# Performance work log

Measured on AMD Instinct MI355X. Metric: run time of the kernel, lower is better.

## Reference

```python
import jax, jax.numpy as jnp
import numpy as np

B, T, IN, CELL, OUT = 512, 32, 512, 128, 128


def setup_inputs() -> dict:
    key = jax.random.key(0)
    ks = jax.random.split(key, 6)
    d = IN + CELL
    w = lambda k, shape, fan: jax.random.normal(k, shape, jnp.float32) / np.sqrt(fan).astype(np.float32)
    return {
        "x": jax.random.normal(ks[0], (B, T, IN), jnp.float32),
        "Wf": w(ks[1], (d, CELL), d), "bf": jnp.zeros((CELL,), jnp.float32),
        "Wi1": w(ks[2], (d, CELL), d), "bi1": jnp.zeros((CELL,), jnp.float32),
        "Wi2": w(ks[3], (d, CELL), d), "bi2": jnp.zeros((CELL,), jnp.float32),
        "Wo": w(ks[4], (d, CELL), d), "bo": jnp.zeros((CELL,), jnp.float32),
        "Wc": w(ks[5], (CELL, OUT), CELL), "bc": jnp.zeros((OUT,), jnp.float32),
    }


def reference(x, Wf, bf, Wi1, bi1, Wi2, bi2, Wo, bo, Wc, bc):
    # Faithful to MyLSTM.forward: loop runs x.shape[1] times; each iteration
    # concatenates the FULL [B,T,CELL] cell_state with the FULL [B,T,IN] x
    # (x is never sliced per step). Only the last iteration's output matters,
    # but we carry it through the scan to match the loop structure exactly.
    Tn = x.shape[1]
    c0 = jnp.zeros(x.shape[:2] + (Wf.shape[1],), x.dtype)
    out0 = jnp.zeros(x.shape[:2] + (Wc.shape[1],), x.dtype)

    def step(carry, _):
        c, _prev_out = carry
        inp = jnp.concatenate([c, x], axis=-1)  # [B,T,CELL+IN]
        f = jax.nn.sigmoid(inp @ Wf + bf)
        c = c * f + jax.nn.sigmoid(inp @ Wi1 + bi1) * jnp.tanh(inp @ Wi2 + bi2)
        o = jax.nn.sigmoid(inp @ Wo + bo) * jnp.tanh(c)
        out = jax.nn.softmax(o @ Wc + bc, axis=2)  # out_features != 1 branch
        return (c, out), None

    (c, out), _ = jax.lax.scan(step, (c0, out0), None, length=Tn)
    return out, c
```

## Files before the change

### kernel.cpp

```cpp
#include <hip/hip_runtime.h>
#include <stdint.h>

#define ROWS  16384
#define CELL  128
#define INF   512
#define RPB   32
#define NSTEP 32

typedef _Float16 f16x8 __attribute__((ext_vector_type(8)));
typedef _Float16 f16x4 __attribute__((ext_vector_type(4)));
typedef float    f32x16 __attribute__((ext_vector_type(16)));

#define MFMA32(a, b, c) __builtin_amdgcn_mfma_f32_32x32x16_f16((a), (b), (c), 0, 0, 0)

#define AOFF  0
#define XOFF  65536
#define WCOFF 327680
#define WSTOT 344064

__device__ __forceinline__ unsigned short f2h_bits(float f) {
  _Float16 h = (_Float16)f;
  return *(unsigned short*)&h;
}
__device__ __forceinline__ float sig_f(float z) {
  return __builtin_amdgcn_rcpf(1.f + __expf(-z));
}
__device__ __forceinline__ float tanh_f(float z) {
  return 1.f - 2.f * __builtin_amdgcn_rcpf(__expf(2.f * z) + 1.f);
}

__global__ __launch_bounds__(256) void prep_kernel(
    const float* __restrict__ Wf, const float* __restrict__ Wi1,
    const float* __restrict__ Wi2, const float* __restrict__ Wo,
    const float* __restrict__ Wc, unsigned short* __restrict__ ws) {
  int id = blockIdx.x * blockDim.x + threadIdx.x;
  if (id >= WSTOT) return;
  const float* Wg[4] = {Wf, Wi1, Wi2, Wo};
  if (id < XOFF) {
    int g = id >> 14, r = id & 16383;
    int j = r & 7, lane = (r >> 3) & 63, tile = r >> 9;
    int nb = tile & 3, ks = tile >> 2;
    int k = ks * 16 + ((lane >> 5) << 3) + j;
    int n = nb * 32 + (lane & 31);
    ws[id] = f2h_bits(Wg[g][k * CELL + n]);
  } else if (id < WCOFF) {
    int t = id - XOFF;
    int g = t >> 16, r = t & 65535;
    int j = r & 7, lane = (r >> 3) & 63, tile = r >> 9;
    int nb = tile & 3, ks = tile >> 2;
    int k = ks * 16 + ((lane >> 5) << 3) + j;
    int n = nb * 32 + (lane & 31);
    ws[id] = f2h_bits(Wg[g][(CELL + k) * CELL + n]);
  } else {
    int r = id - WCOFF;
    int j = r & 7, lane = (r >> 3) & 63, tile = r >> 9;
    int nb = tile & 3, ks = tile >> 2;
    int k = ks * 16 + ((lane >> 5) << 3) + j;
    int n = nb * 32 + (lane & 31);
    ws[id] = f2h_bits(Wc[k * CELL + n]);
  }
}

__global__ __launch_bounds__(256, 2) void lstm_kernel(
    const float* __restrict__ x,
    const float* __restrict__ bf_, const float* __restrict__ bi1,
    const float* __restrict__ bi2, const float* __restrict__ bo,
    const float* __restrict__ bc,
    const unsigned short* __restrict__ ws, float* __restrict__ out) {

  __shared__ union {
    _Float16 xs[32][264];
    struct {
      _Float16 o[32][136];
      float    s[32][132];
    } ep;
  } uS;
  __shared__ _Float16 cF[2][32][136];
  __shared__ float    uo[32][132];

  const int tid  = threadIdx.x;
  const int lane = tid & 63;
  const int w    = tid >> 6;
  const int n    = lane & 31;
  const int l5   = lane >> 5;
  const int col  = w * 32 + n;
  const int r0   = blockIdx.x * RPB;

  const _Float16* Aw  = (const _Float16*)ws + AOFF;
  const _Float16* Xw  = (const _Float16*)ws + XOFF;
  const _Float16* Wcw = (const _Float16*)ws + WCOFF;

  f32x16 u[4];
#pragma unroll
  for (int g = 0; g < 4; ++g)
#pragma unroll
    for (int i = 0; i < 16; ++i) u[g][i] = 0.f;

  const float* xbase = x + (size_t)r0 * INF;
#pragma unroll 1
  for (int ch = 0; ch < 2; ++ch) {
    if (ch) __syncthreads();
#pragma unroll
    for (int i = 0; i < 8; ++i) {
      int flat = tid + i * 256;
      int row = flat >> 6, c4 = flat & 63;
      const float4 v = ((const float4*)(xbase + (size_t)row * INF + ch * 256))[c4];
      f16x4 h = {(_Float16)v.x, (_Float16)v.y, (_Float16)v.z, (_Float16)v.w};
      *(f16x4*)&uS.xs[row][c4 * 4] = h;
    }
    __syncthreads();
#pragma unroll 2
    for (int ks8 = 0; ks8 < 16; ++ks8) {
      f16x8 a = *(const f16x8*)&uS.xs[n][ks8 * 16 + l5 * 8];
      int ks = ch * 16 + ks8;
#pragma unroll
      for (int g = 0; g < 4; ++g) {
        f16x8 b = *(const f16x8*)(Xw + g * 65536 + ((ks * 4 + w) * 64 + lane) * 8);
        u[g] = MFMA32(a, b, u[g]);
      }
    }
  }
  {
    float b0 = bf_[col], b1 = bi1[col], b2 = bi2[col], b3 = bo[col];
#pragma unroll
    for (int reg = 0; reg < 16; ++reg) {
      u[0][reg] += b0; u[1][reg] += b1; u[2][reg] += b2;
      int r = (reg & 3) + 8 * (reg >> 2) + 4 * l5;
      uo[r][col] = u[3][reg] + b3;
    }
  }

  f16x8 wr[3][8];
#pragma unroll
  for (int g = 0; g < 3; ++g)
#pragma unroll
    for (int ks = 0; ks < 8; ++ks)
      wr[g][ks] = *(const f16x8*)(Aw + g * 16384 + ((ks * 4 + w) * 64 + lane) * 8);

  f32x16 cr;
#pragma unroll
  for (int reg = 0; reg < 16; ++reg) {
    float ig = sig_f(u[1][reg]);
    float gg = tanh_f(u[2][reg]);
    float c0 = ig * gg;
    cr[reg] = c0;
    int r = (reg & 3) + 8 * (reg >> 2) + 4 * l5;
    cF[0][r][col] = (_Float16)c0;
  }
  __syncthreads();

#pragma unroll 1
  for (int t = 1; t < NSTEP - 1; ++t) {
    const int rb = (t + 1) & 1, wb = t & 1;
    f16x8 a[8];
#pragma unroll
    for (int ks = 0; ks < 8; ++ks)
      a[ks] = *(const f16x8*)&cF[rb][n][ks * 16 + l5 * 8];
    f32x16 zf = u[0], zi1 = u[1], zi2 = u[2];
#pragma unroll
    for (int ks = 0; ks < 8; ++ks) {
      zf  = MFMA32(a[ks], wr[0][ks], zf);
      zi1 = MFMA32(a[ks], wr[1][ks], zi1);
      zi2 = MFMA32(a[ks], wr[2][ks], zi2);
    }
#pragma unroll
    for (int reg = 0; reg < 16; ++reg) {
      float fg = sig_f(zf[reg]);
      float ig = sig_f(zi1[reg]);
      float gg = tanh_f(zi2[reg]);
      float cn = fmaf(cr[reg], fg, ig * gg);
      cr[reg] = cn;
      int r = (reg & 3) + 8 * (reg >> 2) + 4 * l5;
      cF[wb][r][col] = (_Float16)cn;
    }
    __syncthreads();
  }

  {
    f16x8 a[8];
#pragma unroll
    for (int ks = 0; ks < 8; ++ks)
      a[ks] = *(const f16x8*)&cF[0][n][ks * 16 + l5 * 8];
    f32x16 zf = u[0], zi1 = u[1], zi2 = u[2], zo;
#pragma unroll
    for (int reg = 0; reg < 16; ++reg) {
      int r = (reg & 3) + 8 * (reg >> 2) + 4 * l5;
      zo[reg] = uo[r][col];
    }
#pragma unroll
    for (int ks = 0; ks < 8; ++ks) {
      f16x8 bo_frag = *(const f16x8*)(Aw + 3 * 16384 + ((ks * 4 + w) * 64 + lane) * 8);
      zf  = MFMA32(a[ks], wr[0][ks], zf);
      zi1 = MFMA32(a[ks], wr[1][ks], zi1);
      zi2 = MFMA32(a[ks], wr[2][ks], zi2);
      zo  = MFMA32(a[ks], bo_frag, zo);
    }
    __syncthreads();
#pragma unroll
    for (int reg = 0; reg < 16; ++reg) {
      float fg = sig_f(zf[reg]);
      float ig = sig_f(zi1[reg]);
      float gg = tanh_f(zi2[reg]);
      float cn = fmaf(cr[reg], fg, ig * gg);
      cr[reg] = cn;
      float ov = sig_f(zo[reg]) * tanh_f(cn);
      int r = (reg & 3) + 8 * (reg >> 2) + 4 * l5;
      uS.ep.o[r][col] = (_Float16)ov;
    }
    __syncthreads();
  }

  {
    f32x16 sacc;
#pragma unroll
    for (int i = 0; i < 16; ++i) sacc[i] = 0.f;
#pragma unroll
    for (int ks = 0; ks < 8; ++ks) {
      f16x8 a = *(const f16x8*)&uS.ep.o[n][ks * 16 + l5 * 8];
      f16x8 b = *(const f16x8*)(Wcw + ((ks * 4 + w) * 64 + lane) * 8);
      sacc = MFMA32(a, b, sacc);
    }
    float bv = bc[col];
#pragma unroll
    for (int reg = 0; reg < 16; ++reg) {
      int r = (reg & 3) + 8 * (reg >> 2) + 4 * l5;
      uS.ep.s[r][col] = sacc[reg] + bv;
    }
    __syncthreads();

#pragma unroll
    for (int rr = 0; rr < 8; ++rr) {
      int r = w * 8 + rr;
      float v0 = uS.ep.s[r][lane];
      float v1 = uS.ep.s[r][lane + 64];
      float m = fmaxf(v0, v1);
#pragma unroll
      for (int off = 32; off; off >>= 1) m = fmaxf(m, __shfl_xor(m, off, 64));
      float e0 = __expf(v0 - m), e1 = __expf(v1 - m);
      float sm = e0 + e1;
#pragma unroll
      for (int off = 32; off; off >>= 1) sm += __shfl_xor(sm, off, 64);
      float inv = __builtin_amdgcn_rcpf(sm);
      size_t base = (size_t)(r0 + r) * 128;
      out[base + lane]      = e0 * inv;
      out[base + lane + 64] = e1 * inv;
    }

#pragma unroll
    for (int reg = 0; reg < 16; ++reg) {
      int r = (reg & 3) + 8 * (reg >> 2) + 4 * l5;
      out[(size_t)ROWS * 128 + (size_t)(r0 + r) * 128 + col] = cr[reg];
    }
  }
}

extern "C" void kernel_launch(void* const* d_in, const int* in_sizes, int n_in,
                              void* d_out, int out_size, void* d_ws, size_t ws_size,
                              hipStream_t stream) {
  const float* x   = (const float*)d_in[0];
  const float* Wf  = (const float*)d_in[1];
  const float* bf_ = (const float*)d_in[2];
  const float* Wi1 = (const float*)d_in[3];
  const float* bi1 = (const float*)d_in[4];
  const float* Wi2 = (const float*)d_in[5];
  const float* bi2 = (const float*)d_in[6];
  const float* Wo  = (const float*)d_in[7];
  const float* bo  = (const float*)d_in[8];
  const float* Wc  = (const float*)d_in[9];
  const float* bc  = (const float*)d_in[10];
  unsigned short* ws = (unsigned short*)d_ws;
  float* out = (float*)d_out;

  hipLaunchKernelGGL(prep_kernel, dim3((WSTOT + 255) / 256), dim3(256), 0, stream,
                     Wf, Wi1, Wi2, Wo, Wc, ws);
  hipLaunchKernelGGL(lstm_kernel, dim3(ROWS / RPB), dim3(256), 0, stream,
                     x, bf_, bi1, bi2, bo, bc, ws, out);
}
```

Baseline: 177.4 us.

## Fold exp2 scaling into weights and transpose MFMA operands for vectorized stores

Pre-scales the gate and classifier weights and biases by -log2e or 2*log2e during prep, so activations use raw exp2 and rcp without an extra multiply. Swaps the MFMA operand roles so weights are the A operand and the transposed cell state is B. Each lane's accumulator registers then map to contiguous columns, which allows packed f16x4 and float4 stores to LDS and global memory in place of scalar scattered stores. The uo shared buffer is removed and the output-gate preactivation stays in registers, at the cost of slightly more register pressure and f16 rounding of the scaled weights.

```diff
diff --git a/kernel.cpp b/kernel.cpp
--- a/kernel.cpp
+++ b/kernel.cpp
@@ -7,13 +7,21 @@
 #define RPB   32
 #define NSTEP 32
 
+#define LOG2E 1.4426950408889634f
+
 typedef _Float16 f16x8 __attribute__((ext_vector_type(8)));
 typedef _Float16 f16x4 __attribute__((ext_vector_type(4)));
 typedef float    f32x16 __attribute__((ext_vector_type(16)));
 
 #define MFMA32(a, b, c) __builtin_amdgcn_mfma_f32_32x32x16_f16((a), (b), (c), 0, 0, 0)
 
-#define AOFF  0
+#if __has_builtin(__builtin_amdgcn_exp2f)
+#define EXP2(x) __builtin_amdgcn_exp2f(x)
+#else
+#define EXP2(x) __expf((x) * 0.6931471805599453f)
+#endif
+#define RCP(x) __builtin_amdgcn_rcpf(x)
+
 #define XOFF  65536
 #define WCOFF 327680
 #define WSTOT 344064
@@ -21,12 +29,6 @@
 __device__ __forceinline__ unsigned short f2h_bits(float f) {
   _Float16 h = (_Float16)f;
   return *(unsigned short*)&h;
-}
-__device__ __forceinline__ float sig_f(float z) {
-  return __builtin_amdgcn_rcpf(1.f + __expf(-z));
-}
-__device__ __forceinline__ float tanh_f(float z) {
-  return 1.f - 2.f * __builtin_amdgcn_rcpf(__expf(2.f * z) + 1.f);
 }
 
 __global__ __launch_bounds__(256) void prep_kernel(
@@ -36,28 +38,26 @@
   int id = blockIdx.x * blockDim.x + threadIdx.x;
   if (id >= WSTOT) return;
   const float* Wg[4] = {Wf, Wi1, Wi2, Wo};
+  const float sc[4] = {-LOG2E, -LOG2E, 2.f * LOG2E, -LOG2E};
   if (id < XOFF) {
     int g = id >> 14, r = id & 16383;
-    int j = r & 7, lane = (r >> 3) & 63, tile = r >> 9;
-    int nb = tile & 3, ks = tile >> 2;
+    int w = r >> 12, ks = (r >> 9) & 7, lane = (r >> 3) & 63, j = r & 7;
     int k = ks * 16 + ((lane >> 5) << 3) + j;
-    int n = nb * 32 + (lane & 31);
-    ws[id] = f2h_bits(Wg[g][k * CELL + n]);
+    int n = w * 32 + (lane & 31);
+    ws[id] = f2h_bits(Wg[g][k * CELL + n] * sc[g]);
   } else if (id < WCOFF) {
     int t = id - XOFF;
     int g = t >> 16, r = t & 65535;
-    int j = r & 7, lane = (r >> 3) & 63, tile = r >> 9;
-    int nb = tile & 3, ks = tile >> 2;
+    int w = r >> 14, ks = (r >> 9) & 31, lane = (r >> 3) & 63, j = r & 7;
     int k = ks * 16 + ((lane >> 5) << 3) + j;
-    int n = nb * 32 + (lane & 31);
-    ws[id] = f2h_bits(Wg[g][(CELL + k) * CELL + n]);
+    int n = w * 32 + (lane & 31);
+    ws[id] = f2h_bits(Wg[g][(CELL + k) * CELL + n] * sc[g]);
   } else {
     int r = id - WCOFF;
-    int j = r & 7, lane = (r >> 3) & 63, tile = r >> 9;
-    int nb = tile & 3, ks = tile >> 2;
+    int w = r >> 12, ks = (r >> 9) & 7, lane = (r >> 3) & 63, j = r & 7;
     int k = ks * 16 + ((lane >> 5) << 3) + j;
-    int n = nb * 32 + (lane & 31);
-    ws[id] = f2h_bits(Wc[k * CELL + n]);
+    int n = w * 32 + (lane & 31);
+    ws[id] = f2h_bits(Wc[k * CELL + n] * LOG2E);
   }
 }
 
@@ -75,18 +75,16 @@
       float    s[32][132];
     } ep;
   } uS;
-  __shared__ _Float16 cF[2][32][136];
-  __shared__ float    uo[32][132];
+  __shared__ _Float16 cT[2][32][136];
 
   const int tid  = threadIdx.x;
   const int lane = tid & 63;
   const int w    = tid >> 6;
-  const int n    = lane & 31;
+  const int n31  = lane & 31;
   const int l5   = lane >> 5;
-  const int col  = w * 32 + n;
   const int r0   = blockIdx.x * RPB;
 
-  const _Float16* Aw  = (const _Float16*)ws + AOFF;
+  const _Float16* Aw  = (const _Float16*)ws;
   const _Float16* Xw  = (const _Float16*)ws + XOFF;
   const _Float16* Wcw = (const _Float16*)ws + WCOFF;
 
@@ -110,24 +108,23 @@
     }
     __syncthreads();
 #pragma unroll 2
-    for (int ks8 = 0; ks8 < 16; ++ks8) {
-      f16x8 a = *(const f16x8*)&uS.xs[n][ks8 * 16 + l5 * 8];
-      int ks = ch * 16 + ks8;
+    for (int ksl = 0; ksl < 16; ++ksl) {
+      f16x8 b = *(const f16x8*)&uS.xs[n31][ksl * 16 + l5 * 8];
+      int ks = ch * 16 + ksl;
 #pragma unroll
       for (int g = 0; g < 4; ++g) {
-        f16x8 b = *(const f16x8*)(Xw + g * 65536 + ((ks * 4 + w) * 64 + lane) * 8);
+        f16x8 a = *(const f16x8*)(Xw + (((g * 4 + w) * 32 + ks) * 64 + lane) * 8);
         u[g] = MFMA32(a, b, u[g]);
       }
     }
   }
-  {
-    float b0 = bf_[col], b1 = bi1[col], b2 = bi2[col], b3 = bo[col];
-#pragma unroll
-    for (int reg = 0; reg < 16; ++reg) {
-      u[0][reg] += b0; u[1][reg] += b1; u[2][reg] += b2;
-      int r = (reg & 3) + 8 * (reg >> 2) + 4 * l5;
-      uo[r][col] = u[3][reg] + b3;
-    }
+#pragma unroll
+  for (int reg = 0; reg < 16; ++reg) {
+    int col = w * 32 + (reg & 3) + 8 * (reg >> 2) + 4 * l5;
+    u[0][reg] += bf_[col] * (-LOG2E);
+    u[1][reg] += bi1[col] * (-LOG2E);
+    u[2][reg] += bi2[col] * (2.f * LOG2E);
+    u[3][reg] += bo[col]  * (-LOG2E);
   }
 
   f16x8 wr[3][8];
@@ -135,96 +132,106 @@
   for (int g = 0; g < 3; ++g)
 #pragma unroll
     for (int ks = 0; ks < 8; ++ks)
-      wr[g][ks] = *(const f16x8*)(Aw + g * 16384 + ((ks * 4 + w) * 64 + lane) * 8);
+      wr[g][ks] = *(const f16x8*)(Aw + (((g * 4 + w) * 8 + ks) * 64 + lane) * 8);
 
   f32x16 cr;
 #pragma unroll
   for (int reg = 0; reg < 16; ++reg) {
-    float ig = sig_f(u[1][reg]);
-    float gg = tanh_f(u[2][reg]);
-    float c0 = ig * gg;
-    cr[reg] = c0;
-    int r = (reg & 3) + 8 * (reg >> 2) + 4 * l5;
-    cF[0][r][col] = (_Float16)c0;
+    float ig = RCP(1.f + EXP2(u[1][reg]));
+    float gg = fmaf(-2.f, RCP(1.f + EXP2(u[2][reg])), 1.f);
+    cr[reg] = ig * gg;
+  }
+#pragma unroll
+  for (int qd = 0; qd < 4; ++qd) {
+    f16x4 p = {(_Float16)cr[qd * 4 + 0], (_Float16)cr[qd * 4 + 1],
+               (_Float16)cr[qd * 4 + 2], (_Float16)cr[qd * 4 + 3]};
+    *(f16x4*)&cT[0][n31][w * 32 + qd * 8 + l5 * 4] = p;
   }
   __syncthreads();
 
 #pragma unroll 1
   for (int t = 1; t < NSTEP - 1; ++t) {
     const int rb = (t + 1) & 1, wb = t & 1;
-    f16x8 a[8];
+    f16x8 b[8];
 #pragma unroll
     for (int ks = 0; ks < 8; ++ks)
-      a[ks] = *(const f16x8*)&cF[rb][n][ks * 16 + l5 * 8];
+      b[ks] = *(const f16x8*)&cT[rb][n31][ks * 16 + l5 * 8];
     f32x16 zf = u[0], zi1 = u[1], zi2 = u[2];
 #pragma unroll
     for (int ks = 0; ks < 8; ++ks) {
-      zf  = MFMA32(a[ks], wr[0][ks], zf);
-      zi1 = MFMA32(a[ks], wr[1][ks], zi1);
-      zi2 = MFMA32(a[ks], wr[2][ks], zi2);
+      zf  = MFMA32(wr[0][ks], b[ks], zf);
+      zi1 = MFMA32(wr[1][ks], b[ks], zi1);
+      zi2 = MFMA32(wr[2][ks], b[ks], zi2);
     }
 #pragma unroll
     for (int reg = 0; reg < 16; ++reg) {
-      float fg = sig_f(zf[reg]);
-      float ig = sig_f(zi1[reg]);
-      float gg = tanh_f(zi2[reg]);
+      float fg = RCP(1.f + EXP2(zf[reg]));
+      float ig = RCP(1.f + EXP2(zi1[reg]));
+      float gg = fmaf(-2.f, RCP(1.f + EXP2(zi2[reg])), 1.f);
+      cr[reg] = fmaf(cr[reg], fg, ig * gg);
+    }
+#pragma unroll
+    for (int qd = 0; qd < 4; ++qd) {
+      f16x4 p = {(_Float16)cr[qd * 4 + 0], (_Float16)cr[qd * 4 + 1],
+                 (_Float16)cr[qd * 4 + 2], (_Float16)cr[qd * 4 + 3]};
+      *(f16x4*)&cT[wb][n31][w * 32 + qd * 8 + l5 * 4] = p;
+    }
+    __syncthreads();
+  }
+
+  {
+    f16x8 b[8];
+#pragma unroll
+    for (int ks = 0; ks < 8; ++ks)
+      b[ks] = *(const f16x8*)&cT[0][n31][ks * 16 + l5 * 8];
+    f32x16 zf = u[0], zi1 = u[1], zi2 = u[2], zo = u[3];
+#pragma unroll
+    for (int ks = 0; ks < 8; ++ks) {
+      f16x8 wof = *(const f16x8*)(Aw + (((3 * 4 + w) * 8 + ks) * 64 + lane) * 8);
+      zf  = MFMA32(wr[0][ks], b[ks], zf);
+      zi1 = MFMA32(wr[1][ks], b[ks], zi1);
+      zi2 = MFMA32(wr[2][ks], b[ks], zi2);
+      zo  = MFMA32(wof, b[ks], zo);
+    }
+    float ovv[16];
+#pragma unroll
+    for (int reg = 0; reg < 16; ++reg) {
+      float fg = RCP(1.f + EXP2(zf[reg]));
+      float ig = RCP(1.f + EXP2(zi1[reg]));
+      float gg = fmaf(-2.f, RCP(1.f + EXP2(zi2[reg])), 1.f);
       float cn = fmaf(cr[reg], fg, ig * gg);
       cr[reg] = cn;
-      int r = (reg & 3) + 8 * (reg >> 2) + 4 * l5;
-      cF[wb][r][col] = (_Float16)cn;
+      float th = fmaf(-2.f, RCP(1.f + EXP2(cn * (2.f * LOG2E))), 1.f);
+      ovv[reg] = RCP(1.f + EXP2(zo[reg])) * th;
+    }
+#pragma unroll
+    for (int qd = 0; qd < 4; ++qd) {
+      f16x4 p = {(_Float16)ovv[qd * 4 + 0], (_Float16)ovv[qd * 4 + 1],
+                 (_Float16)ovv[qd * 4 + 2], (_Float16)ovv[qd * 4 + 3]};
+      *(f16x4*)&uS.ep.o[n31][w * 32 + qd * 8 + l5 * 4] = p;
     }
     __syncthreads();
   }
 
   {
-    f16x8 a[8];
-#pragma unroll
-    for (int ks = 0; ks < 8; ++ks)
-      a[ks] = *(const f16x8*)&cF[0][n][ks * 16 + l5 * 8];
-    f32x16 zf = u[0], zi1 = u[1], zi2 = u[2], zo;
+    f32x16 sa;
+#pragma unroll
+    for (int i = 0; i < 16; ++i) sa[i] = 0.f;
+#pragma unroll
+    for (int ks = 0; ks < 8; ++ks) {
+      f16x8 a = *(const f16x8*)(Wcw + ((w * 8 + ks) * 64 + lane) * 8);
+      f16x8 b = *(const f16x8*)&uS.ep.o[n31][ks * 16 + l5 * 8];
+      sa = MFMA32(a, b, sa);
+    }
 #pragma unroll
     for (int reg = 0; reg < 16; ++reg) {
-      int r = (reg & 3) + 8 * (reg >> 2) + 4 * l5;
-      zo[reg] = uo[r][col];
-    }
-#pragma unroll
-    for (int ks = 0; ks < 8; ++ks) {
-      f16x8 bo_frag = *(const f16x8*)(Aw + 3 * 16384 + ((ks * 4 + w) * 64 + lane) * 8);
-      zf  = MFMA32(a[ks], wr[0][ks], zf);
-      zi1 = MFMA32(a[ks], wr[1][ks], zi1);
-      zi2 = MFMA32(a[ks], wr[2][ks], zi2);
-      zo  = MFMA32(a[ks], bo_frag, zo);
-    }
-    __syncthreads();
-#pragma unroll
-    for (int reg = 0; reg < 16; ++reg) {
-      float fg = sig_f(zf[reg]);
-      float ig = sig_f(zi1[reg]);
-      float gg = tanh_f(zi2[reg]);
-      float cn = fmaf(cr[reg], fg, ig * gg);
-      cr[reg] = cn;
-      float ov = sig_f(zo[reg]) * tanh_f(cn);
-      int r = (reg & 3) + 8 * (reg >> 2) + 4 * l5;
-      uS.ep.o[r][col] = (_Float16)ov;
-    }
-    __syncthreads();
-  }
-
-  {
-    f32x16 sacc;
-#pragma unroll
-    for (int i = 0; i < 16; ++i) sacc[i] = 0.f;
-#pragma unroll
-    for (int ks = 0; ks < 8; ++ks) {
-      f16x8 a = *(const f16x8*)&uS.ep.o[n][ks * 16 + l5 * 8];
-      f16x8 b = *(const f16x8*)(Wcw + ((ks * 4 + w) * 64 + lane) * 8);
-      sacc = MFMA32(a, b, sacc);
-    }
-    float bv = bc[col];
-#pragma unroll
-    for (int reg = 0; reg < 16; ++reg) {
-      int r = (reg & 3) + 8 * (reg >> 2) + 4 * l5;
-      uS.ep.s[r][col] = sacc[reg] + bv;
+      int col = w * 32 + (reg & 3) + 8 * (reg >> 2) + 4 * l5;
+      sa[reg] += bc[col] * LOG2E;
+    }
+#pragma unroll
+    for (int qd = 0; qd < 4; ++qd) {
+      float4 p = {sa[qd * 4 + 0], sa[qd * 4 + 1], sa[qd * 4 + 2], sa[qd * 4 + 3]};
+      *(float4*)&uS.ep.s[n31][w * 32 + qd * 8 + l5 * 4] = p;
     }
     __syncthreads();
 
@@ -236,20 +243,21 @@
       float m = fmaxf(v0, v1);
 #pragma unroll
       for (int off = 32; off; off >>= 1) m = fmaxf(m, __shfl_xor(m, off, 64));
-      float e0 = __expf(v0 - m), e1 = __expf(v1 - m);
+      float e0 = EXP2(v0 - m), e1 = EXP2(v1 - m);
       float sm = e0 + e1;
 #pragma unroll
       for (int off = 32; off; off >>= 1) sm += __shfl_xor(sm, off, 64);
-      float inv = __builtin_amdgcn_rcpf(sm);
+      float inv = RCP(sm);
       size_t base = (size_t)(r0 + r) * 128;
       out[base + lane]      = e0 * inv;
       out[base + lane + 64] = e1 * inv;
     }
 
 #pragma unroll
-    for (int reg = 0; reg < 16; ++reg) {
-      int r = (reg & 3) + 8 * (reg >> 2) + 4 * l5;
-      out[(size_t)ROWS * 128 + (size_t)(r0 + r) * 128 + col] = cr[reg];
+    for (int qd = 0; qd < 4; ++qd) {
+      float4 p = {cr[qd * 4 + 0], cr[qd * 4 + 1], cr[qd * 4 + 2], cr[qd * 4 + 3]};
+      *(float4*)&out[(size_t)ROWS * 128 + (size_t)(r0 + n31) * 128 +
+                     w * 32 + qd * 8 + l5 * 4] = p;
     }
   }
 }
```

After: 178.9 us. About the same (+0.9%).
